# Kernel optimization log

Hardware: AMD Instinct MI355X
Metric: run time of the kernel (lower is better)

## Reference

```python
import jax, jax.numpy as jnp
import numpy as np

EMBED_DIM = 2048
NUM_HEADS = 32
NUM_SEQS = 8
SEQ_LEN = 1024
TOTAL_TOKENS = NUM_SEQS * SEQ_LEN


def setup_inputs() -> dict:
    key = jax.random.key(0)
    ks = jax.random.split(key, 9)
    E = EMBED_DIM
    std = 0.02
    return {
        "hidden_states": jax.random.normal(ks[0], (TOTAL_TOKENS, E), dtype=jnp.float32),
        "Wq": jax.random.normal(ks[1], (E, E), dtype=jnp.float32) * std,
        "bq": jax.random.normal(ks[2], (E,), dtype=jnp.float32) * std,
        "Wk": jax.random.normal(ks[3], (E, E), dtype=jnp.float32) * std,
        "bk": jax.random.normal(ks[4], (E,), dtype=jnp.float32) * std,
        "Wv": jax.random.normal(ks[5], (E, E), dtype=jnp.float32) * std,
        "bv": jax.random.normal(ks[6], (E,), dtype=jnp.float32) * std,
        "Wo": jax.random.normal(ks[7], (E, E), dtype=jnp.float32) * std,
        "bo": jax.random.normal(ks[8], (E,), dtype=jnp.float32) * std,
        "seq_len": SEQ_LEN,
    }


def reference(hidden_states, Wq, bq, Wk, bk, Wv, bv, Wo, bo, seq_len):
    # OPTAttention (has_cache=False): block-diagonal causal attention over
    # packed ragged sequences; here all NUM_SEQS sequences have length seq_len,
    # so the block-diagonal mask is exactly per-sequence causal attention.
    T, E = hidden_states.shape
    H = NUM_HEADS
    D = E // H
    B = T // seq_len
    scaling = D ** -0.5

    # torch nn.Linear: y = x @ W.T + b
    q = hidden_states @ Wq.T + bq
    k = hidden_states @ Wk.T + bk
    v = hidden_states @ Wv.T + bv

    q = q.reshape(B, seq_len, H, D)
    k = k.reshape(B, seq_len, H, D)
    v = v.reshape(B, seq_len, H, D)

    # [B, H, S, S] attention scores (xformers applies scale to q@k.T)
    scores = jnp.einsum("bqhd,bkhd->bhqk", q, k) * scaling
    causal = jnp.tril(jnp.ones((seq_len, seq_len), dtype=bool))
    scores = jnp.where(causal[None, None, :, :], scores, jnp.finfo(scores.dtype).min)
    probs = jax.nn.softmax(scores, axis=-1)

    attn = jnp.einsum("bhqk,bkhd->bqhd", probs, v)  # [B, S, H, D]
    attn = attn.reshape(T, E)
    return attn @ Wo.T + bo
```

## Files before the change

kernel.cpp:

```cpp
#include <hip/hip_runtime.h>
#include <hip/hip_bf16.h>

typedef __bf16 bf16_t;
typedef __bf16 bf16x8 __attribute__((ext_vector_type(8)));
typedef __bf16 bf16x4 __attribute__((ext_vector_type(4)));
typedef float f32x4 __attribute__((ext_vector_type(4)));
typedef float f32x16 __attribute__((ext_vector_type(16)));
typedef unsigned short u16x8 __attribute__((ext_vector_type(8)));
typedef unsigned int u32x4 __attribute__((ext_vector_type(4)));

#define T_TOK 8192
#define E_DIM 2048
#define NHEAD 32
#define SEQLEN 1024
#define NSEQ 8
#define LDQ 6144

#if __has_builtin(__builtin_amdgcn_exp2f)
#define EXP2F(x) __builtin_amdgcn_exp2f(x)
#else
#define EXP2F(x) exp2f(x)
#endif

static __device__ inline unsigned cvtpk_bf16(float lo, float hi) {
    unsigned r;
    asm("v_cvt_pk_bf16_f32 %0, %1, %2" : "=v"(r) : "v"(lo), "v"(hi));
    return r;
}

static __device__ inline void plswap(unsigned &x, unsigned &y, bool lo_half) {
#if __has_builtin(__builtin_amdgcn_permlane32_swap)
    auto r = __builtin_amdgcn_permlane32_swap(x, y, false, false);
    x = r[0]; y = r[1];
#else
    unsigned xs = __shfl_xor(x, 32), ys = __shfl_xor(y, 32);
    unsigned nx = lo_half ? x : ys;
    unsigned ny = lo_half ? xs : y;
    x = nx; y = ny;
#endif
}

__global__ void cvt_f32_bf16(const float* __restrict__ in, bf16_t* __restrict__ out, int n4) {
    int idx = blockIdx.x * blockDim.x + threadIdx.x;
    int stride = gridDim.x * blockDim.x;
    for (int i = idx; i < n4; i += stride) {
        const float4 v = reinterpret_cast<const float4*>(in)[i];
        bf16x4 o;
        o[0] = (bf16_t)v.x; o[1] = (bf16_t)v.y; o[2] = (bf16_t)v.z; o[3] = (bf16_t)v.w;
        reinterpret_cast<bf16x4*>(out)[i] = o;
    }
}

template<bool OUT_BF16>
__global__ __launch_bounds__(512, 2)
void gemm256(const bf16_t* __restrict__ A, const bf16_t* __restrict__ B,
             const float* __restrict__ b0, const float* __restrict__ b1,
             const float* __restrict__ b2, void* __restrict__ Cout,
             int M, int N, int K, float qs, int qlim) {
    __shared__ alignas(16) unsigned char lds[65536];
    const int tid = threadIdx.x;
    const int wid = tid >> 6, l = tid & 63;
    const int cpx = gridDim.x >> 3;
    const int wg = (blockIdx.x & 7) * cpx + (blockIdx.x >> 3);
    const int nbm = M >> 8;
    const int bm = wg % nbm, bn = wg / nbm;
    const int wrow = (wid >> 2) * 128, wcol = (wid & 3) * 64;
    const int lr = l & 15, lg = l >> 4;

    f32x4 acc[8][4] = {};

    const int sr = l >> 2;
    const int scb = (l & 3) * 16;
    const bf16_t* aBase = A + (size_t)(bm * 256) * K;
    const bf16_t* bBase = B + (size_t)(bn * 256) * K;

    auto stage = [&](int kt, int b) {
        unsigned char* base = lds + b * 32768;
#pragma unroll
        for (int c = 0; c < 2; ++c) {
            const int r = (wid * 2 + c) * 16 + sr;
            const int cbs = scb ^ (((r >> 1) & 3) << 4);
            __builtin_amdgcn_global_load_lds(
                (const __attribute__((address_space(1))) void*)(aBase + (size_t)r * K + kt * 32 + (cbs >> 1)),
                (__attribute__((address_space(3))) void*)(base + (wid * 2 + c) * 1024), 16, 0, 0);
            __builtin_amdgcn_global_load_lds(
                (const __attribute__((address_space(1))) void*)(bBase + (size_t)r * K + kt * 32 + (cbs >> 1)),
                (__attribute__((address_space(3))) void*)(base + 16384 + (wid * 2 + c) * 1024), 16, 0, 0);
        }
    };

    const int nk = K >> 5;
    stage(0, 0);
    stage(1, 1);
    asm volatile("s_waitcnt vmcnt(4)" ::: "memory");
    __builtin_amdgcn_s_barrier();

    int b = 0;
    for (int kt = 0; kt < nk; ++kt) {
        const unsigned char* Ab = lds + b * 32768;
        bf16x8 af[8], bfv[4];
#pragma unroll
        for (int m = 0; m < 8; ++m) {
            const int r = wrow + m * 16 + lr;
            const int cb = (lg * 16) ^ (((r >> 1) & 3) << 4);
            af[m] = *reinterpret_cast<const bf16x8*>(Ab + r * 64 + cb);
        }
#pragma unroll
        for (int n = 0; n < 4; ++n) {
            const int r = wcol + n * 16 + lr;
            const int cb = (lg * 16) ^ (((r >> 1) & 3) << 4);
            bfv[n] = *reinterpret_cast<const bf16x8*>(Ab + 16384 + r * 64 + cb);
        }
        __builtin_amdgcn_s_setprio(1);
#pragma unroll
        for (int m = 0; m < 8; ++m)
#pragma unroll
            for (int n = 0; n < 4; ++n)
                acc[m][n] = __builtin_amdgcn_mfma_f32_16x16x32_bf16(af[m], bfv[n], acc[m][n], 0, 0, 0);
        __builtin_amdgcn_s_setprio(0);
        if (kt == nk - 1) break;
        asm volatile("s_waitcnt lgkmcnt(0)" ::: "memory");
        __builtin_amdgcn_sched_barrier(0);
        __builtin_amdgcn_s_barrier();
        if (kt + 2 < nk) {
            stage(kt + 2, b);
            asm volatile("s_waitcnt vmcnt(4)" ::: "memory");
        } else {
            asm volatile("s_waitcnt vmcnt(0)" ::: "memory");
        }
        __builtin_amdgcn_s_barrier();
        b ^= 1;
    }

    const int r0 = bm * 256 + wrow + lg * 4;
    const int c0 = bn * 256 + wcol + lr;
#pragma unroll
    for (int n = 0; n < 4; ++n) {
        const int cc = c0 + n * 16;
        const float bias = (cc < 2048) ? b0[cc] : (cc < 4096 ? b1[cc - 2048] : b2[cc - 4096]);
        const float sc = (cc < qlim) ? qs : 1.0f;
#pragma unroll
        for (int m = 0; m < 8; ++m)
#pragma unroll
            for (int j = 0; j < 4; ++j) {
                const int rr = r0 + m * 16 + j;
                const float v = (acc[m][n][j] + bias) * sc;
                if (OUT_BF16) ((bf16_t*)Cout)[(size_t)rr * N + cc] = (bf16_t)v;
                else          ((float*)Cout)[(size_t)rr * N + cc] = v;
            }
    }
}

__global__ __launch_bounds__(512, 2)
void attn_fwd3(const bf16_t* __restrict__ QKV, bf16_t* __restrict__ Og) {
    const int orig = blockIdx.x;
    const int id = (orig & 7) * 64 + (orig >> 3);
    const int grp = id >> 1;
    const int pairIdx = id & 1;
    const int h = grp & 31;
    const int sq = grp >> 5;

    const int tid = threadIdx.x;
    const int w = tid >> 6;
    const int l = tid & 63;
    const int ll = l & 31;
    const int hi = l >> 5;
    const bool lo_half = (hi == 0);

    __shared__ alignas(16) unsigned char lds[65536];

    const bf16_t* Qg = QKV;
    const bf16_t* Kg = QKV + 2048;
    const bf16_t* Vg = QKV + 4096;
    const size_t kvbase = (size_t)(sq * SEQLEN) * LDQ + h * 64;

    bf16x8 vr0, vr1;
    const int vk0 = l * 2;
    const int vd0 = w * 8;

    auto stageK = [&](int kt, int buf) {
#pragma unroll
        for (int c = 0; c < 2; ++c) {
            const int o = (w * 2 + c) * 1024 + l * 16;
            const int r = o >> 7;
            const int swb = (o & 127) ^ ((r & 7) << 4);
            const bf16_t* src = Kg + kvbase + (size_t)(kt * 128 + r) * LDQ + (swb >> 1);
            __builtin_amdgcn_global_load_lds(
                (const __attribute__((address_space(1))) void*)src,
                (__attribute__((address_space(3))) void*)(lds + buf * 16384 + (w * 2 + c) * 1024),
                16, 0, 0);
        }
    };
    auto loadV = [&](int kt) {
        const bf16_t* vp = Vg + kvbase + (size_t)(kt * 128 + vk0) * LDQ + vd0;
        vr0 = *reinterpret_cast<const bf16x8*>(vp);
        vr1 = *reinterpret_cast<const bf16x8*>(vp + LDQ);
    };
    auto writeV = [&](int buf) {
        u16x8 s0 = __builtin_bit_cast(u16x8, vr0);
        u16x8 s1 = __builtin_bit_cast(u16x8, vr1);
        unsigned char* vb = lds + 32768 + buf * 16384;
#pragma unroll
        for (int e = 0; e < 8; ++e) {
            const int d = vd0 + e;
            unsigned off = (unsigned)(d * 256 + vk0 * 2);
            off ^= ((unsigned)((d ^ (d >> 4)) & 15)) << 4;
            *reinterpret_cast<unsigned*>(vb + off) = (unsigned)s0[e] | ((unsigned)s1[e] << 16);
        }
    };

    const unsigned ksw = (unsigned)((l & 7) << 4);
    const unsigned kbase = (unsigned)(ll * 128 + hi * 16);

#pragma unroll 1
    for (int seg = 0; seg < 2; ++seg) {
        const int qt = pairIdx ? (seg ? 2 : 1) : (seg ? 3 : 0);

        const int q_glob = qt * 256 + w * 32 + ll;
        const bf16_t* qp = Qg + (size_t)(sq * SEQLEN + q_glob) * LDQ + h * 64 + hi * 8;
        bf16x8 qf[4];
#pragma unroll
        for (int dc = 0; dc < 4; ++dc)
            qf[dc] = *reinterpret_cast<const bf16x8*>(qp + dc * 16);

        const int nkt = 2 * qt + 2;
        const int q_wave_max = qt * 256 + w * 32 + 31;

        f32x16 oac[2] = {};
        float mrun = -3.0e38f, lsum = 0.f;

        stageK(0, 0);
        loadV(0);
        writeV(0);
        __syncthreads();

        int cur = 0;
        for (int kt = 0; kt < nkt; ++kt) {
            const bool notlast = (kt + 1 < nkt);
            if (notlast) { stageK(kt + 1, cur ^ 1); loadV(kt + 1); }

            if (kt * 128 <= q_wave_max) {
                const unsigned char* Kcur = lds + cur * 16384;
                const unsigned char* Vcur = lds + 32768 + cur * 16384;

                f32x16 st[4];
#pragma unroll
                for (int kh = 0; kh < 4; ++kh) {
                    f32x16 acc = {};
#pragma unroll
                    for (int dc = 0; dc < 4; ++dc) {
                        const unsigned off = (kbase + (unsigned)(kh * 4096 + dc * 32)) ^ ksw;
                        const bf16x8 ka = *reinterpret_cast<const bf16x8*>(Kcur + off);
                        acc = __builtin_amdgcn_mfma_f32_32x32x16_bf16(ka, qf[dc], acc, 0, 0, 0);
                    }
                    st[kh] = acc;
                }

                if (kt >= 2 * qt) {
#pragma unroll
                    for (int kh = 0; kh < 4; ++kh)
#pragma unroll
                        for (int r = 0; r < 16; ++r) {
                            const int kg = kt * 128 + kh * 32 + (r & 3) + 8 * (r >> 2) + 4 * hi;
                            if (kg > q_glob) st[kh][r] = -3.0e38f;
                        }
                }

                float tm = -3.0e38f;
#pragma unroll
                for (int kh = 0; kh < 4; ++kh)
#pragma unroll
                    for (int r = 0; r < 16; ++r) tm = fmaxf(tm, st[kh][r]);
                tm = fmaxf(tm, __shfl_xor(tm, 32));

                if (!__all(tm <= mrun + 8.0f)) {
                    const float mnew = fmaxf(mrun, tm);
                    const float rsc = EXP2F(mrun - mnew);
                    mrun = mnew;
                    lsum *= rsc;
#pragma unroll
                    for (int dh = 0; dh < 2; ++dh)
#pragma unroll
                        for (int r = 0; r < 16; ++r) oac[dh][r] *= rsc;
                }

                float ps = 0.f;
#pragma unroll
                for (int kh = 0; kh < 4; ++kh)
#pragma unroll
                    for (int r = 0; r < 16; ++r) {
                        const float p = EXP2F(st[kh][r] - mrun);
                        st[kh][r] = p;
                        ps += p;
                    }
                ps += __shfl_xor(ps, 32);
                lsum += ps;

                bf16x8 pf[8];
#pragma unroll
                for (int kh = 0; kh < 4; ++kh)
#pragma unroll
                    for (int hc = 0; hc < 2; ++hc) {
                        const int b0i = hc * 8;
                        unsigned a  = cvtpk_bf16(st[kh][b0i + 0], st[kh][b0i + 1]);
                        unsigned b  = cvtpk_bf16(st[kh][b0i + 4], st[kh][b0i + 5]);
                        unsigned a2 = cvtpk_bf16(st[kh][b0i + 2], st[kh][b0i + 3]);
                        unsigned b2 = cvtpk_bf16(st[kh][b0i + 6], st[kh][b0i + 7]);
                        plswap(a, b, lo_half);
                        plswap(a2, b2, lo_half);
                        u32x4 words = { a, a2, b, b2 };
                        pf[kh * 2 + hc] = __builtin_bit_cast(bf16x8, words);
                    }

#pragma unroll
                for (int dh = 0; dh < 2; ++dh) {
                    const int d = dh * 32 + ll;
                    const unsigned vsw = ((unsigned)((d ^ (d >> 4)) & 15)) << 4;
                    const unsigned vbb = (unsigned)(d * 256 + hi * 16);
#pragma unroll
                    for (int kc = 0; kc < 8; ++kc) {
                        const unsigned off = (vbb + (unsigned)(kc * 32)) ^ vsw;
                        const bf16x8 vfr = *reinterpret_cast<const bf16x8*>(Vcur + off);
                        oac[dh] = __builtin_amdgcn_mfma_f32_32x32x16_bf16(vfr, pf[kc], oac[dh], 0, 0, 0);
                    }
                }
            }

            if (notlast) writeV(cur ^ 1);
            __syncthreads();
            cur ^= 1;
        }

        const float inv = 1.0f / lsum;
        bf16_t* op = Og + (size_t)(sq * SEQLEN + q_glob) * E_DIM + h * 64;
#pragma unroll
        for (int dh = 0; dh < 2; ++dh)
#pragma unroll
            for (int rq = 0; rq < 4; ++rq) {
                const int d0 = dh * 32 + 8 * rq + 4 * hi;
                bf16x4 ov;
#pragma unroll
                for (int j = 0; j < 4; ++j)
                    ov[j] = (bf16_t)(oac[dh][rq * 4 + j] * inv);
                *reinterpret_cast<bf16x4*>(op + d0) = ov;
            }
    }
}

extern "C" void kernel_launch(void* const* d_in, const int* in_sizes, int n_in,
                              void* d_out, int out_size, void* d_ws, size_t ws_size,
                              hipStream_t stream) {
    const float* hid = (const float*)d_in[0];
    const float* Wq  = (const float*)d_in[1];
    const float* bq  = (const float*)d_in[2];
    const float* Wk  = (const float*)d_in[3];
    const float* bk  = (const float*)d_in[4];
    const float* Wv  = (const float*)d_in[5];
    const float* bv  = (const float*)d_in[6];
    const float* Wo  = (const float*)d_in[7];
    const float* bo  = (const float*)d_in[8];
    float* out = (float*)d_out;

    const size_t TE = (size_t)T_TOK * E_DIM;
    const size_t EE = (size_t)E_DIM * E_DIM;

    bf16_t* ws   = (bf16_t*)d_ws;
    bf16_t* hidB = ws;
    bf16_t* qkvB = ws + TE;
    bf16_t* Wcat = qkvB + 3 * TE;
    bf16_t* WoB  = Wcat + 3 * EE;

    cvt_f32_bf16<<<2048, 256, 0, stream>>>(hid, hidB, (int)(TE / 4));
    cvt_f32_bf16<<<1024, 256, 0, stream>>>(Wq, Wcat, (int)(EE / 4));
    cvt_f32_bf16<<<1024, 256, 0, stream>>>(Wk, Wcat + EE, (int)(EE / 4));
    cvt_f32_bf16<<<1024, 256, 0, stream>>>(Wv, Wcat + 2 * EE, (int)(EE / 4));
    cvt_f32_bf16<<<1024, 256, 0, stream>>>(Wo, WoB, (int)(EE / 4));

    const float QSCALE = 0.125f * 1.4426950408889634f;

    gemm256<true><<<dim3((T_TOK / 256) * (LDQ / 256)), 512, 0, stream>>>(
        hidB, Wcat, bq, bk, bv, qkvB, T_TOK, LDQ, E_DIM, QSCALE, 2048);

    attn_fwd3<<<dim3(512), 512, 0, stream>>>(qkvB, hidB);

    gemm256<false><<<dim3((T_TOK / 256) * (E_DIM / 256)), 512, 0, stream>>>(
        hidB, WoB, bo, bo, bo, out, T_TOK, E_DIM, E_DIM, 1.0f, 0);
}
```

Measured before the change: 413.6 us.

## Deepen GEMM pipeline to four LDS stages with split A/B prefetch

Reworks the 256x256 GEMM main loop to use a 4-deep LDS ring (128KB) with three tiles in flight, instead of double buffering. Each k-step is split into two MFMA halves, with the A and B prefetches for a later tile issued between them so loads overlap compute. K is also made a compile-time constant. Using 128KB of LDS per block likely drops occupancy from the requested 2 blocks per CU to 1, and the extra barriers add synchronisation cost.

```diff
diff --git a/kernel.cpp b/kernel.cpp
--- a/kernel.cpp
+++ b/kernel.cpp
@@ -53,11 +53,13 @@
 
 template<bool OUT_BF16>
 __global__ __launch_bounds__(512, 2)
-void gemm256(const bf16_t* __restrict__ A, const bf16_t* __restrict__ B,
-             const float* __restrict__ b0, const float* __restrict__ b1,
-             const float* __restrict__ b2, void* __restrict__ Cout,
-             int M, int N, int K, float qs, int qlim) {
-    __shared__ alignas(16) unsigned char lds[65536];
+void gemm256p(const bf16_t* __restrict__ A, const bf16_t* __restrict__ B,
+              const float* __restrict__ b0, const float* __restrict__ b1,
+              const float* __restrict__ b2, void* __restrict__ Cout,
+              int M, int N, float qs, int qlim) {
+    constexpr int K = 2048;
+    constexpr int NK = K / 32;
+    __shared__ alignas(16) unsigned char lds[131072];
     const int tid = threadIdx.x;
     const int wid = tid >> 6, l = tid & 63;
     const int cpx = gridDim.x >> 3;
@@ -69,67 +71,87 @@
 
     f32x4 acc[8][4] = {};
 
-    const int sr = l >> 2;
-    const int scb = (l & 3) * 16;
     const bf16_t* aBase = A + (size_t)(bm * 256) * K;
     const bf16_t* bBase = B + (size_t)(bn * 256) * K;
-
-    auto stage = [&](int kt, int b) {
-        unsigned char* base = lds + b * 32768;
+    const int sr = l >> 2;
+    const int sc = (l & 3) * 16;
+
+    auto stageA = [&](int t) {
+        unsigned char* base = lds + (t & 3) * 32768;
 #pragma unroll
         for (int c = 0; c < 2; ++c) {
-            const int r = (wid * 2 + c) * 16 + sr;
-            const int cbs = scb ^ (((r >> 1) & 3) << 4);
+            const int chunk = wid * 2 + c;
+            const int r = chunk * 16 + sr;
+            const int cb = sc ^ (((r >> 1) & 3) << 4);
             __builtin_amdgcn_global_load_lds(
-                (const __attribute__((address_space(1))) void*)(aBase + (size_t)r * K + kt * 32 + (cbs >> 1)),
-                (__attribute__((address_space(3))) void*)(base + (wid * 2 + c) * 1024), 16, 0, 0);
+                (const __attribute__((address_space(1))) void*)(aBase + (size_t)r * K + t * 32 + (cb >> 1)),
+                (__attribute__((address_space(3))) void*)(base + chunk * 1024), 16, 0, 0);
+        }
+    };
+    auto stageB = [&](int t) {
+        unsigned char* base = lds + (t & 3) * 32768 + 16384;
+#pragma unroll
+        for (int c = 0; c < 2; ++c) {
+            const int chunk = wid * 2 + c;
+            const int r = chunk * 16 + sr;
+            const int cb = sc ^ (((r >> 1) & 3) << 4);
             __builtin_amdgcn_global_load_lds(
-                (const __attribute__((address_space(1))) void*)(bBase + (size_t)r * K + kt * 32 + (cbs >> 1)),
-                (__attribute__((address_space(3))) void*)(base + 16384 + (wid * 2 + c) * 1024), 16, 0, 0);
+                (const __attribute__((address_space(1))) void*)(bBase + (size_t)r * K + t * 32 + (cb >> 1)),
+                (__attribute__((address_space(3))) void*)(base + chunk * 1024), 16, 0, 0);
         }
     };
 
-    const int nk = K >> 5;
-    stage(0, 0);
-    stage(1, 1);
-    asm volatile("s_waitcnt vmcnt(4)" ::: "memory");
+    stageA(0); stageB(0); stageA(1); stageB(1); stageA(2); stageB(2);
+    asm volatile("s_waitcnt vmcnt(8)" ::: "memory");
     __builtin_amdgcn_s_barrier();
 
-    int b = 0;
-    for (int kt = 0; kt < nk; ++kt) {
-        const unsigned char* Ab = lds + b * 32768;
+    for (int t = 0; t < NK; ++t) {
+        const unsigned char* Ab = lds + (t & 3) * 32768;
+        const unsigned char* Bb = Ab + 16384;
         bf16x8 af[8], bfv[4];
 #pragma unroll
-        for (int m = 0; m < 8; ++m) {
+        for (int m = 0; m < 4; ++m) {
             const int r = wrow + m * 16 + lr;
-            const int cb = (lg * 16) ^ (((r >> 1) & 3) << 4);
-            af[m] = *reinterpret_cast<const bf16x8*>(Ab + r * 64 + cb);
+            af[m] = *reinterpret_cast<const bf16x8*>(Ab + r * 64 + ((lg * 16) ^ (((r >> 1) & 3) << 4)));
         }
 #pragma unroll
         for (int n = 0; n < 4; ++n) {
             const int r = wcol + n * 16 + lr;
-            const int cb = (lg * 16) ^ (((r >> 1) & 3) << 4);
-            bfv[n] = *reinterpret_cast<const bf16x8*>(Ab + 16384 + r * 64 + cb);
-        }
+            bfv[n] = *reinterpret_cast<const bf16x8*>(Bb + r * 64 + ((lg * 16) ^ (((r >> 1) & 3) << 4)));
+        }
+        if (t + 3 < NK) stageA(t + 3);
+        __builtin_amdgcn_s_barrier();
+        asm volatile("s_waitcnt lgkmcnt(0)" ::: "memory");
+        __builtin_amdgcn_sched_barrier(0);
         __builtin_amdgcn_s_setprio(1);
 #pragma unroll
-        for (int m = 0; m < 8; ++m)
+        for (int m = 0; m < 4; ++m)
 #pragma unroll
             for (int n = 0; n < 4; ++n)
                 acc[m][n] = __builtin_amdgcn_mfma_f32_16x16x32_bf16(af[m], bfv[n], acc[m][n], 0, 0, 0);
         __builtin_amdgcn_s_setprio(0);
-        if (kt == nk - 1) break;
+        __builtin_amdgcn_s_barrier();
+#pragma unroll
+        for (int m = 4; m < 8; ++m) {
+            const int r = wrow + m * 16 + lr;
+            af[m] = *reinterpret_cast<const bf16x8*>(Ab + r * 64 + ((lg * 16) ^ (((r >> 1) & 3) << 4)));
+        }
+        if (t + 3 < NK) stageB(t + 3);
+        __builtin_amdgcn_s_barrier();
         asm volatile("s_waitcnt lgkmcnt(0)" ::: "memory");
         __builtin_amdgcn_sched_barrier(0);
+        __builtin_amdgcn_s_setprio(1);
+#pragma unroll
+        for (int m = 4; m < 8; ++m)
+#pragma unroll
+            for (int n = 0; n < 4; ++n)
+                acc[m][n] = __builtin_amdgcn_mfma_f32_16x16x32_bf16(af[m], bfv[n], acc[m][n], 0, 0, 0);
+        __builtin_amdgcn_s_setprio(0);
+        if (t == NK - 1) break;
+        if (t <= NK - 4)      asm volatile("s_waitcnt vmcnt(8)" ::: "memory");
+        else if (t == NK - 3) asm volatile("s_waitcnt vmcnt(4)" ::: "memory");
+        else                  asm volatile("s_waitcnt vmcnt(0)" ::: "memory");
         __builtin_amdgcn_s_barrier();
-        if (kt + 2 < nk) {
-            stage(kt + 2, b);
-            asm volatile("s_waitcnt vmcnt(4)" ::: "memory");
-        } else {
-            asm volatile("s_waitcnt vmcnt(0)" ::: "memory");
-        }
-        __builtin_amdgcn_s_barrier();
-        b ^= 1;
     }
 
     const int r0 = bm * 256 + wrow + lg * 4;
@@ -138,13 +160,13 @@
     for (int n = 0; n < 4; ++n) {
         const int cc = c0 + n * 16;
         const float bias = (cc < 2048) ? b0[cc] : (cc < 4096 ? b1[cc - 2048] : b2[cc - 4096]);
-        const float sc = (cc < qlim) ? qs : 1.0f;
+        const float sc2 = (cc < qlim) ? qs : 1.0f;
 #pragma unroll
         for (int m = 0; m < 8; ++m)
 #pragma unroll
             for (int j = 0; j < 4; ++j) {
                 const int rr = r0 + m * 16 + j;
-                const float v = (acc[m][n][j] + bias) * sc;
+                const float v = (acc[m][n][j] + bias) * sc2;
                 if (OUT_BF16) ((bf16_t*)Cout)[(size_t)rr * N + cc] = (bf16_t)v;
                 else          ((float*)Cout)[(size_t)rr * N + cc] = v;
             }
@@ -378,11 +400,11 @@
 
     const float QSCALE = 0.125f * 1.4426950408889634f;
 
-    gemm256<true><<<dim3((T_TOK / 256) * (LDQ / 256)), 512, 0, stream>>>(
-        hidB, Wcat, bq, bk, bv, qkvB, T_TOK, LDQ, E_DIM, QSCALE, 2048);
+    gemm256p<true><<<dim3((T_TOK / 256) * (LDQ / 256)), 512, 0, stream>>>(
+        hidB, Wcat, bq, bk, bv, qkvB, T_TOK, LDQ, QSCALE, 2048);
 
     attn_fwd3<<<dim3(512), 512, 0, stream>>>(qkvB, hidB);
 
-    gemm256<false><<<dim3((T_TOK / 256) * (E_DIM / 256)), 512, 0, stream>>>(
-        hidB, WoB, bo, bo, bo, out, T_TOK, E_DIM, E_DIM, 1.0f, 0);
-}
+    gemm256p<false><<<dim3((T_TOK / 256) * (E_DIM / 256)), 512, 0, stream>>>(
+        hidB, WoB, bo, bo, bo, out, T_TOK, E_DIM, 1.0f, 0);
+}
```

After: 412.5 us. No clear change (-0.2%).
